# Performance work log

Measured on AMD Instinct MI355X. Metric: run time of the kernel, lower is better.

Reference implementation:

```python
import jax, jax.numpy as jnp
import numpy as np

H = 2048          # hidden_size
I = 8192          # intermediate_size (shared expert)
E = 32            # num_experts
K = 4             # num_experts_per_tok
M = 1408          # moe_intermediate_size
B, S = 2, 1024


def setup_inputs() -> dict:
    key = jax.random.key(0)
    ks = jax.random.split(key, 7)
    scale = 0.02
    return {
        "hidden_states": jax.random.normal(ks[0], (B, S, H), dtype=jnp.float32),
        "gate_w": jax.random.normal(ks[1], (H, E), dtype=jnp.float32) * scale,
        "w1": jax.random.normal(ks[2], (E, H, M), dtype=jnp.float32) * scale,  # expert up-proj
        "w2": jax.random.normal(ks[3], (E, M, H), dtype=jnp.float32) * scale,  # expert down-proj
        "ws1": jax.random.normal(ks[4], (H, I), dtype=jnp.float32) * scale,    # shared up-proj
        "ws2": jax.random.normal(ks[5], (I, H), dtype=jnp.float32) * scale,    # shared down-proj
    }


def reference(hidden_states, gate_w, w1, w2, ws1, ws2):
    b, s, h = hidden_states.shape
    x = hidden_states.reshape(-1, h)                      # [T, H]

    # shared expert: Linear -> SiLU -> Linear
    shared = jax.nn.silu(x @ ws1) @ ws2                   # [T, H]

    # router: top-k logits, softmax over the k selected logits
    router_logits = x @ gate_w                            # [T, E]
    top_vals, top_idx = jax.lax.top_k(router_logits, K)   # [T, K]
    routing_weights = jax.nn.softmax(top_vals, axis=-1)   # [T, K]

    # combine weights: scatter top-k weights into dense [T, E]
    cw = (jax.nn.one_hot(top_idx, E, dtype=x.dtype)
          * routing_weights[..., None]).sum(axis=1)       # [T, E]

    # expert FFNs (dense over experts, weighted combine)
    a = jax.nn.silu(jnp.einsum('th,ehm->tem', x, w1))     # [T, E, M]
    expert_out = jnp.einsum('tem,emh,te->th', a, w2, cw)  # [T, H]

    output = (shared + expert_out).reshape(b, s, h)
    return output, router_logits.reshape(b, s, E)
```

## Files before the change

kernel.cpp:

```cpp
#include <hip/hip_runtime.h>

#define H_ 2048
#define E_ 32
#define KSEL 4
#define M_ 1408
#define I_ 8192
#define T_ 2048

typedef __bf16 bf16;
typedef bf16 bf16x8 __attribute__((ext_vector_type(8)));
typedef float f32x4 __attribute__((ext_vector_type(4)));
typedef unsigned short u16x8 __attribute__((ext_vector_type(8)));
typedef unsigned int u32x4 __attribute__((ext_vector_type(4)));

static __device__ __forceinline__ unsigned short bfb(float f) {
  return __builtin_bit_cast(unsigned short, (bf16)f);
}

static __device__ __forceinline__ void gload_lds16(const void* g, void* l) {
  __builtin_amdgcn_global_load_lds((const __attribute__((address_space(1))) void*)g,
                                   (__attribute__((address_space(3))) void*)l, 16, 0, 0);
}

static __device__ __forceinline__ float silu_f(float v) {
  return v / (1.f + __expf(-v));
}

static __device__ __forceinline__ void wave_argmax(float& v, int& vi) {
  #pragma unroll
  for (int off = 32; off >= 1; off >>= 1) {
    float ov = __shfl_xor(v, off);
    int   oi = __shfl_xor(vi, off);
    if (ov > v || (ov == v && oi < vi)) { v = ov; vi = oi; }
  }
}

__global__ __launch_bounds__(64) void prep_k(int* __restrict__ counts) {
  if (threadIdx.x < E_) counts[threadIdx.x] = 0;
}

__global__ __launch_bounds__(256) void cvt_k(const float* __restrict__ x, unsigned short* __restrict__ xb) {
  size_t i = ((size_t)blockIdx.x * 256 + threadIdx.x) * 8;
  float4 a = *(const float4*)(x + i);
  float4 b = *(const float4*)(x + i + 4);
  u16x8 o;
  o[0]=bfb(a.x); o[1]=bfb(a.y); o[2]=bfb(a.z); o[3]=bfb(a.w);
  o[4]=bfb(b.x); o[5]=bfb(b.y); o[6]=bfb(b.z); o[7]=bfb(b.w);
  *(u16x8*)(xb + i) = o;
}

__global__ __launch_bounds__(256) void combine_k(const float* __restrict__ sc,
                                                 const float* __restrict__ sc2,
                                                 float* __restrict__ out) {
  size_t i = ((size_t)blockIdx.x * 256 + threadIdx.x) * 4;
  int t = (int)(i >> 11);
  int h = (int)(i & 2047);
  const float* s = sc + (size_t)(t * 4) * H_ + h;
  float4 a = *(const float4*)(s);
  float4 b = *(const float4*)(s + H_);
  float4 c = *(const float4*)(s + 2 * H_);
  float4 d = *(const float4*)(s + 3 * H_);
  float4 o;
  o.x = a.x + b.x + c.x + d.x;
  o.y = a.y + b.y + c.y + d.y;
  o.z = a.z + b.z + c.z + d.z;
  o.w = a.w + b.w + c.w + d.w;
  #pragma unroll
  for (int kz = 0; kz < 4; ++kz) {
    float4 v = *(const float4*)(sc2 + (size_t)kz * T_ * H_ + i);
    o.x += v.x; o.y += v.y; o.z += v.z; o.w += v.w;
  }
  *(float4*)(out + i) = o;
}

__global__ __launch_bounds__(64) void router_k(const float* __restrict__ x, const float* __restrict__ gw,
                                               float* __restrict__ logits, int* __restrict__ counts,
                                               int* __restrict__ tlist, float* __restrict__ wlist) {
  int t = blockIdx.x;
  int l = threadIdx.x;
  int e = l & 31;
  int half = l >> 5;
  const float* xr = x + (size_t)t * H_ + half * (H_/2);
  const float* g  = gw + (size_t)(half * (H_/2)) * E_ + e;
  float a0=0.f, a1=0.f, a2=0.f, a3=0.f;
  for (int h = 0; h < H_/2; h += 4) {
    a0 = fmaf(xr[h],   g[(size_t)h*E_],     a0);
    a1 = fmaf(xr[h+1], g[(size_t)(h+1)*E_], a1);
    a2 = fmaf(xr[h+2], g[(size_t)(h+2)*E_], a2);
    a3 = fmaf(xr[h+3], g[(size_t)(h+3)*E_], a3);
  }
  float acc = (a0+a1)+(a2+a3);
  acc += __shfl_xor(acc, 32);
  if (l < E_) logits[(size_t)t*E_ + l] = acc;

  float cur = (l < E_) ? acc : -INFINITY;
  int myidx = (l < E_) ? e : 1000;
  float tv0,tv1,tv2,tv3; int ti0,ti1,ti2,ti3;
  { float v=cur; int vi=myidx; wave_argmax(v,vi); tv0=v; ti0=vi; if (myidx==vi) cur=-INFINITY; }
  { float v=cur; int vi=myidx; wave_argmax(v,vi); tv1=v; ti1=vi; if (myidx==vi) cur=-INFINITY; }
  { float v=cur; int vi=myidx; wave_argmax(v,vi); tv2=v; ti2=vi; if (myidx==vi) cur=-INFINITY; }
  { float v=cur; int vi=myidx; wave_argmax(v,vi); tv3=v; ti3=vi; }
  float w0 = 1.f;
  float w1 = __expf(tv1 - tv0);
  float w2 = __expf(tv2 - tv0);
  float w3 = __expf(tv3 - tv0);
  float inv = 1.f / (w0+w1+w2+w3);
  if (l < KSEL) {
    float myw = ((l==0)?w0:(l==1)?w1:(l==2)?w2:w3) * inv;
    int   myi = ((l==0)?ti0:(l==1)?ti1:(l==2)?ti2:ti3);
    int pos = atomicAdd(&counts[myi], 1);
    tlist[myi*T_ + pos] = (t << 2) | l;
    wlist[myi*T_ + pos] = myw;
  }
}

template<int MODE, int KDIM, int NDIM, int ASTR, int KSPLIT>
__global__ __launch_bounds__(256) void gemm_k(
    const bf16* __restrict__ A, const float* __restrict__ Bf,
    bf16* __restrict__ Cb, float* __restrict__ Cf,
    const int* __restrict__ tlist, const float* __restrict__ wlist,
    const int* __restrict__ counts)
{
  __shared__ __align__(16) char smem[24576];
  char* As = smem;
  char* Bs = smem + 16384;
  const int tid = threadIdx.x;

  int mt, nt, e = 0, kz = 0;
  int nrows = T_;
  const int* lst = nullptr;
  const float* Bp = Bf;
  if constexpr (MODE == 2 || MODE == 3) {
    constexpr int NT = NDIM / 64;
    constexpr int NWG = NT * E_ * 2;
    constexpr int CPX = NWG / 8;
    int id = blockIdx.x;
    int lg = (id & 7) * CPX + (id >> 3);
    int bit = lg & 1;
    int en  = lg >> 1;
    e  = en / NT;
    nt = en % NT;
    mt = (blockIdx.y == 0) ? bit : (2 + 2*((int)blockIdx.y - 1) + bit);
    nrows = counts[e];
    if (mt * 128 >= nrows) return;
    lst = tlist + e*T_;
    Bp = Bf + (size_t)e * ((size_t)KDIM * NDIM);
  } else {
    constexpr int NWG = 16 * (NDIM / 64);
    constexpr int CPX = NWG / 8;
    int id = blockIdx.x;
    int lg = (id & 7) * CPX + (id >> 3);
    mt = lg & 15;
    nt = lg >> 4;
    if constexpr (KSPLIT > 1) kz = blockIdx.z;
  }
  const int mrow0 = mt*128, ncol0 = nt*64;

  const bf16* abase[4];
  int aoffs[4];
  #pragma unroll
  for (int c = 0; c < 4; ++c) {
    int lidx = c*256 + tid;
    int row  = lidx >> 3;
    int slot = lidx & 7;
    aoffs[c] = (slot ^ (row & 7)) * 8;
    int ri = mrow0 + row;
    if constexpr (MODE == 2) {
      int tt = (ri < nrows) ? (lst[ri] >> 2) : 0;
      abase[c] = A + (size_t)tt * ASTR;
    } else if constexpr (MODE == 3) {
      int ar = (ri < nrows) ? lst[ri] : 0;
      abase[c] = A + (size_t)ar * ASTR;
    } else {
      abase[c] = A + (size_t)ri * ASTR;
    }
  }

  const int bn = tid & 63;
  const int bq = tid >> 6;
  const float* bsrc0 = Bp + (size_t)(bq * 16) * NDIM + ncol0 + bn;
  char* const bdst = Bs + (bq*2)*1024 + bn*16;

  const int l  = tid & 63;
  const int wv = tid >> 6;
  const int wr = wv >> 1, wc = wv & 1;
  const int ss = l >> 4;

  f32x4 acc[4][2] = {};

  constexpr int ITERS = KDIM / 64 / KSPLIT;
  static_assert(ITERS % 2 == 0, "K-loop is 2-unrolled");
  const int kt0 = kz * ITERS;
  const int ktend = kt0 + ITERS;

  float vA[16], vB[16];

#define LOADB(P, KT) do {                                            \
    const float* bs_ = bsrc0 + (size_t)((KT) * 64) * NDIM;           \
    _Pragma("unroll")                                                \
    for (int j = 0; j < 16; ++j) P[j] = bs_[(size_t)j * NDIM];       \
  } while (0)

#define WRITEB(P) do {                                               \
    u32x4 lo_, hi_;                                                  \
    _Pragma("unroll")                                                \
    for (int j = 0; j < 4; ++j) {                                    \
      lo_[j] = (unsigned)bfb(P[2*j])   | ((unsigned)bfb(P[2*j+1]) << 16); \
      hi_[j] = (unsigned)bfb(P[8+2*j]) | ((unsigned)bfb(P[8+2*j+1]) << 16); \
    }                                                                \
    *(u32x4*)(bdst)        = lo_;                                    \
    *(u32x4*)(bdst + 1024) = hi_;                                    \
  } while (0)

#define MFMA_HALF(S) do {                                            \
    bf16x8 af[4], bfr[2];                                            \
    const int ks = (S)*4 + ss;                                       \
    _Pragma("unroll")                                                \
    for (int mf = 0; mf < 4; ++mf) {                                 \
      int r = wr*64 + mf*16 + (l & 15);                              \
      af[mf] = *(const bf16x8*)(As + r*128 + ((ks ^ (r & 7)) << 4)); \
    }                                                                \
    _Pragma("unroll")                                                \
    for (int nf = 0; nf < 2; ++nf) {                                 \
      int c = wc*32 + nf*16 + (l & 15);                              \
      bfr[nf] = *(const bf16x8*)(Bs + ks*1024 + c*16);               \
    }                                                                \
    _Pragma("unroll")                                                \
    for (int mf = 0; mf < 4; ++mf)                                   \
      _Pragma("unroll")                                              \
      for (int nf = 0; nf < 2; ++nf)                                 \
        acc[mf][nf] = __builtin_amdgcn_mfma_f32_16x16x32_bf16(af[mf], bfr[nf], acc[mf][nf], 0, 0, 0); \
  } while (0)

#define MFMA_PHASE() do { MFMA_HALF(0); MFMA_HALF(1); } while (0)

#define ADMA(KT) do {                                                \
    _Pragma("unroll")                                                \
    for (int c = 0; c < 4; ++c)                                      \
      gload_lds16(abase[c] + (KT)*64 + aoffs[c], As + (c*256 + tid)*16); \
  } while (0)

  LOADB(vA, kt0);
  for (int kt = kt0; kt < ktend; kt += 2) {
    __syncthreads();
    ADMA(kt);
    WRITEB(vA);
    __syncthreads();
    LOADB(vB, kt + 1);
    MFMA_PHASE();

    __syncthreads();
    ADMA(kt + 1);
    WRITEB(vB);
    __syncthreads();
    if (kt + 2 < ktend) LOADB(vA, kt + 2);
    MFMA_PHASE();
  }

#undef LOADB
#undef WRITEB
#undef MFMA_HALF
#undef MFMA_PHASE
#undef ADMA

  #pragma unroll
  for (int mf = 0; mf < 4; ++mf) {
    #pragma unroll
    for (int j = 0; j < 4; ++j) {
      const int rloc = wr*64 + mf*16 + (l >> 4)*4 + j;
      const int grow = mrow0 + rloc;
      if constexpr (MODE == 0) {
        #pragma unroll
        for (int nf = 0; nf < 2; ++nf) {
          int col = ncol0 + wc*32 + nf*16 + (l & 15);
          Cb[(size_t)grow * NDIM + col] = (bf16)silu_f(acc[mf][nf][j]);
        }
      } else if constexpr (MODE == 1) {
        float* dst = Cf + (size_t)kz * T_ * H_;
        #pragma unroll
        for (int nf = 0; nf < 2; ++nf) {
          int col = ncol0 + wc*32 + nf*16 + (l & 15);
          dst[(size_t)grow * NDIM + col] = acc[mf][nf][j];
        }
      } else if constexpr (MODE == 2) {
        if (grow < nrows) {
          int entry = lst[grow];
          float wg = wlist[e*T_ + grow];
          #pragma unroll
          for (int nf = 0; nf < 2; ++nf) {
            int col = ncol0 + wc*32 + nf*16 + (l & 15);
            Cb[(size_t)entry * NDIM + col] = (bf16)(silu_f(acc[mf][nf][j]) * wg);
          }
        }
      } else {
        if (grow < nrows) {
          int entry = lst[grow];
          #pragma unroll
          for (int nf = 0; nf < 2; ++nf) {
            int col = ncol0 + wc*32 + nf*16 + (l & 15);
            Cf[(size_t)entry * H_ + col] = acc[mf][nf][j];
          }
        }
      }
    }
  }
}

extern "C" void kernel_launch(void* const* d_in, const int* in_sizes, int n_in,
                              void* d_out, int out_size, void* d_ws, size_t ws_size,
                              hipStream_t stream) {
  const float* x   = (const float*)d_in[0];
  const float* gw  = (const float*)d_in[1];
  const float* w1  = (const float*)d_in[2];
  const float* w2  = (const float*)d_in[3];
  const float* ws1 = (const float*)d_in[4];
  const float* ws2 = (const float*)d_in[5];
  float* out    = (float*)d_out;
  float* logits = out + (size_t)T_ * H_;

  char* ws = (char*)d_ws;
  const size_t off_xb   = 0;
  const size_t off_y1   = off_xb  + (size_t)T_ * H_ * 2;
  const size_t off_act  = off_y1  + (size_t)T_ * I_ * 2;
  const size_t off_cnt  = off_act + (size_t)T_ * 4 * M_ * 2;
  const size_t off_tl   = off_cnt + 256;
  const size_t off_wl   = off_tl  + (size_t)E_ * T_ * 4;
  const size_t off_sc   = off_wl  + (size_t)E_ * T_ * 4;
  const size_t off_sc2  = off_sc  + (size_t)T_ * 4 * H_ * 4;

  const bf16* xb = (const bf16*)(ws + off_xb);
  bf16* y1  = (bf16*)(ws + off_y1);
  bf16* act = (bf16*)(ws + off_act);
  int*  counts = (int*)(ws + off_cnt);
  int*  tlist  = (int*)(ws + off_tl);
  float* wlist = (float*)(ws + off_wl);
  float* scratch  = (float*)(ws + off_sc);
  float* scratch2 = (float*)(ws + off_sc2);

  prep_k<<<1, 64, 0, stream>>>(counts);
  router_k<<<T_, 64, 0, stream>>>(x, gw, logits, counts, tlist, wlist);
  cvt_k<<<2048, 256, 0, stream>>>(x, (unsigned short*)(ws + off_xb));

  gemm_k<0, 2048, 8192, 2048, 1><<<dim3(2048), 256, 0, stream>>>(
      xb, ws1, y1, nullptr, nullptr, nullptr, nullptr);
  gemm_k<1, 8192, 2048, 8192, 4><<<dim3(512, 1, 4), 256, 0, stream>>>(
      y1, ws2, nullptr, scratch2, nullptr, nullptr, nullptr);
  gemm_k<2, 2048, 1408, 2048, 1><<<dim3(22*E_*2, 8), 256, 0, stream>>>(
      xb, w1, act, nullptr, tlist, wlist, counts);
  gemm_k<3, 1408, 2048, 1408, 1><<<dim3(32*E_*2, 8), 256, 0, stream>>>(
      act, w2, nullptr, scratch, tlist, nullptr, counts);
  combine_k<<<4096, 256, 0, stream>>>(scratch, scratch2, out);
}
```

Baseline: 807.6 us.

## Stream fp32 B tiles into LDS via async DMA and convert to bf16 there

Replaces per-thread register loads of the fp32 weight tile with global_load_lds direct-to-LDS DMA into a double-buffered fp32 staging area. Each thread then reads its column from LDS, converts it to bf16 and writes the swizzled bf16 tile that the MFMA path reads. The aim is to cut VGPR pressure and let weight loads overlap with compute asynchronously. In exchange, LDS per block grows from 24KB to 56KB, which can lower occupancy, and each tile now takes an extra LDS round-trip.

```diff
diff --git a/kernel.cpp b/kernel.cpp
--- a/kernel.cpp
+++ b/kernel.cpp
@@ -121,9 +121,10 @@
     const int* __restrict__ tlist, const float* __restrict__ wlist,
     const int* __restrict__ counts)
 {
-  __shared__ __align__(16) char smem[24576];
-  char* As = smem;
-  char* Bs = smem + 16384;
+  __shared__ __align__(16) char smem[57344];
+  char* As   = smem;
+  char* Bs32 = smem + 16384;
+  char* Bsb  = smem + 49152;
   const int tid = threadIdx.x;
 
   int mt, nt, e = 0, kz = 0;
@@ -176,10 +177,16 @@
     }
   }
 
+  const float* bbaseD[4];
+  #pragma unroll
+  for (int c = 0; c < 4; ++c) {
+    int lidx = c*256 + tid;
+    bbaseD[c] = Bp + (size_t)(lidx >> 4) * NDIM + ncol0 + (lidx & 15) * 4;
+  }
+
   const int bn = tid & 63;
   const int bq = tid >> 6;
-  const float* bsrc0 = Bp + (size_t)(bq * 16) * NDIM + ncol0 + bn;
-  char* const bdst = Bs + (bq*2)*1024 + bn*16;
+  char* const bdst = Bsb + (bq*2)*1024 + bn*16;
 
   const int l  = tid & 63;
   const int wv = tid >> 6;
@@ -193,20 +200,30 @@
   const int kt0 = kz * ITERS;
   const int ktend = kt0 + ITERS;
 
-  float vA[16], vB[16];
-
-#define LOADB(P, KT) do {                                            \
-    const float* bs_ = bsrc0 + (size_t)((KT) * 64) * NDIM;           \
-    _Pragma("unroll")                                                \
-    for (int j = 0; j < 16; ++j) P[j] = bs_[(size_t)j * NDIM];       \
+#define ADMA(KT) do {                                                \
+    _Pragma("unroll")                                                \
+    for (int c = 0; c < 4; ++c)                                      \
+      gload_lds16(abase[c] + (KT)*64 + aoffs[c], As + (c*256 + tid)*16); \
   } while (0)
 
-#define WRITEB(P) do {                                               \
+#define BDMA(KT, BUF) do {                                           \
+    _Pragma("unroll")                                                \
+    for (int c = 0; c < 4; ++c)                                      \
+      gload_lds16(bbaseD[c] + (size_t)(KT)*64*NDIM,                  \
+                  Bs32 + (BUF)*16384 + (c*256 + tid)*16);            \
+  } while (0)
+
+#define CVT(BUF) do {                                                \
+    const char* b32_ = Bs32 + (BUF)*16384;                           \
+    float f_[16];                                                    \
+    _Pragma("unroll")                                                \
+    for (int j = 0; j < 16; ++j)                                     \
+      f_[j] = *(const float*)(b32_ + (bq*16 + j)*256 + bn*4);        \
     u32x4 lo_, hi_;                                                  \
     _Pragma("unroll")                                                \
     for (int j = 0; j < 4; ++j) {                                    \
-      lo_[j] = (unsigned)bfb(P[2*j])   | ((unsigned)bfb(P[2*j+1]) << 16); \
-      hi_[j] = (unsigned)bfb(P[8+2*j]) | ((unsigned)bfb(P[8+2*j+1]) << 16); \
+      lo_[j] = (unsigned)bfb(f_[2*j])   | ((unsigned)bfb(f_[2*j+1]) << 16); \
+      hi_[j] = (unsigned)bfb(f_[8+2*j]) | ((unsigned)bfb(f_[8+2*j+1]) << 16); \
     }                                                                \
     *(u32x4*)(bdst)        = lo_;                                    \
     *(u32x4*)(bdst + 1024) = hi_;                                    \
@@ -223,7 +240,7 @@
     _Pragma("unroll")                                                \
     for (int nf = 0; nf < 2; ++nf) {                                 \
       int c = wc*32 + nf*16 + (l & 15);                              \
-      bfr[nf] = *(const bf16x8*)(Bs + ks*1024 + c*16);               \
+      bfr[nf] = *(const bf16x8*)(Bsb + ks*1024 + c*16);              \
     }                                                                \
     _Pragma("unroll")                                                \
     for (int mf = 0; mf < 4; ++mf)                                   \
@@ -234,34 +251,30 @@
 
 #define MFMA_PHASE() do { MFMA_HALF(0); MFMA_HALF(1); } while (0)
 
-#define ADMA(KT) do {                                                \
-    _Pragma("unroll")                                                \
-    for (int c = 0; c < 4; ++c)                                      \
-      gload_lds16(abase[c] + (KT)*64 + aoffs[c], As + (c*256 + tid)*16); \
-  } while (0)
-
-  LOADB(vA, kt0);
+  BDMA(kt0, 0);
+  __syncthreads();
+
   for (int kt = kt0; kt < ktend; kt += 2) {
     __syncthreads();
     ADMA(kt);
-    WRITEB(vA);
+    BDMA(kt + 1, 1);
+    CVT(0);
     __syncthreads();
-    LOADB(vB, kt + 1);
     MFMA_PHASE();
 
     __syncthreads();
     ADMA(kt + 1);
-    WRITEB(vB);
+    if (kt + 2 < ktend) BDMA(kt + 2, 0);
+    CVT(1);
     __syncthreads();
-    if (kt + 2 < ktend) LOADB(vA, kt + 2);
     MFMA_PHASE();
   }
 
-#undef LOADB
-#undef WRITEB
+#undef ADMA
+#undef BDMA
+#undef CVT
 #undef MFMA_HALF
 #undef MFMA_PHASE
-#undef ADMA
 
   #pragma unroll
   for (int mf = 0; mf < 4; ++mf) {
```

Measured after the change: 845.3 us. +4.7%, slower.

## Merge shared-expert and routed-expert GEMMs into two combined launches

Applied to the files above, without the earlier changes.

Four separate GEMM launches are replaced by two kernels. Each kernel dispatches on block index to either the routed-expert GEMM or the shared-expert GEMM of the same stage. Blocks from the two independent GEMMs can then co-run, filling the tail idle time and the many early-exit expert blocks left by sparse routing. The cost is fixed grid shapes and a possible mismatch between work ordering and block scheduling.

```diff
diff --git a/kernel.cpp b/kernel.cpp
--- a/kernel.cpp
+++ b/kernel.cpp
@@ -115,45 +115,15 @@
 }
 
 template<int MODE, int KDIM, int NDIM, int ASTR, int KSPLIT>
-__global__ __launch_bounds__(256) void gemm_k(
-    const bf16* __restrict__ A, const float* __restrict__ Bf,
+__device__ __forceinline__ void gemm_body(
+    char* __restrict__ smem, int mt, int nt, int kz, int nrows,
+    const bf16* __restrict__ A, const float* __restrict__ Bp,
     bf16* __restrict__ Cb, float* __restrict__ Cf,
-    const int* __restrict__ tlist, const float* __restrict__ wlist,
-    const int* __restrict__ counts)
+    const int* __restrict__ lst, const float* __restrict__ wl)
 {
-  __shared__ __align__(16) char smem[24576];
   char* As = smem;
   char* Bs = smem + 16384;
   const int tid = threadIdx.x;
-
-  int mt, nt, e = 0, kz = 0;
-  int nrows = T_;
-  const int* lst = nullptr;
-  const float* Bp = Bf;
-  if constexpr (MODE == 2 || MODE == 3) {
-    constexpr int NT = NDIM / 64;
-    constexpr int NWG = NT * E_ * 2;
-    constexpr int CPX = NWG / 8;
-    int id = blockIdx.x;
-    int lg = (id & 7) * CPX + (id >> 3);
-    int bit = lg & 1;
-    int en  = lg >> 1;
-    e  = en / NT;
-    nt = en % NT;
-    mt = (blockIdx.y == 0) ? bit : (2 + 2*((int)blockIdx.y - 1) + bit);
-    nrows = counts[e];
-    if (mt * 128 >= nrows) return;
-    lst = tlist + e*T_;
-    Bp = Bf + (size_t)e * ((size_t)KDIM * NDIM);
-  } else {
-    constexpr int NWG = 16 * (NDIM / 64);
-    constexpr int CPX = NWG / 8;
-    int id = blockIdx.x;
-    int lg = (id & 7) * CPX + (id >> 3);
-    mt = lg & 15;
-    nt = lg >> 4;
-    if constexpr (KSPLIT > 1) kz = blockIdx.z;
-  }
   const int mrow0 = mt*128, ncol0 = nt*64;
 
   const bf16* abase[4];
@@ -285,7 +255,7 @@
       } else if constexpr (MODE == 2) {
         if (grow < nrows) {
           int entry = lst[grow];
-          float wg = wlist[e*T_ + grow];
+          float wg = wl[grow];
           #pragma unroll
           for (int nf = 0; nf < 2; ++nf) {
             int col = ncol0 + wc*32 + nf*16 + (l & 15);
@@ -306,6 +276,73 @@
   }
 }
 
+__global__ __launch_bounds__(256) void fusedA_k(
+    const bf16* __restrict__ xb, const float* __restrict__ w1, const float* __restrict__ ws1,
+    bf16* __restrict__ act, bf16* __restrict__ y1,
+    const int* __restrict__ tlist, const float* __restrict__ wlist, const int* __restrict__ counts)
+{
+  __shared__ __align__(16) char smem[24576];
+  if (blockIdx.x < 1408) {
+    constexpr int NT = M_ / 64;
+    constexpr int NWG = NT * E_ * 2;
+    constexpr int CPX = NWG / 8;
+    int id = blockIdx.x;
+    int lg = (id & 7) * CPX + (id >> 3);
+    int bit = lg & 1;
+    int en  = lg >> 1;
+    int e  = en / NT;
+    int nt = en % NT;
+    int mt = (blockIdx.y == 0) ? bit : (2 + 2*((int)blockIdx.y - 1) + bit);
+    int nrows = counts[e];
+    if (mt * 128 >= nrows) return;
+    gemm_body<2, 2048, M_, 2048, 1>(smem, mt, nt, 0, nrows,
+        xb, w1 + (size_t)e * 2048 * M_, act, nullptr, tlist + e*T_, wlist + e*T_);
+  } else {
+    int t = ((int)blockIdx.x - 1408) * 8 + (int)blockIdx.y;
+    constexpr int CPX = 2048 / 8;
+    int lg = (t & 7) * CPX + (t >> 3);
+    int mt = lg & 15;
+    int nt = lg >> 4;
+    gemm_body<0, 2048, I_, 2048, 1>(smem, mt, nt, 0, T_,
+        xb, ws1, y1, nullptr, nullptr, nullptr);
+  }
+}
+
+__global__ __launch_bounds__(256) void fusedB_k(
+    const bf16* __restrict__ y1, const float* __restrict__ ws2,
+    const bf16* __restrict__ act, const float* __restrict__ w2,
+    float* __restrict__ scratch2, float* __restrict__ scratch,
+    const int* __restrict__ tlist, const int* __restrict__ counts)
+{
+  __shared__ __align__(16) char smem[24576];
+  if (blockIdx.x < 2048) {
+    constexpr int NT = H_ / 64;
+    constexpr int NWG = NT * E_ * 2;
+    constexpr int CPX = NWG / 8;
+    int id = blockIdx.x;
+    int lg = (id & 7) * CPX + (id >> 3);
+    int bit = lg & 1;
+    int en  = lg >> 1;
+    int e  = en / NT;
+    int nt = en % NT;
+    int mt = (blockIdx.y == 0) ? bit : (2 + 2*((int)blockIdx.y - 1) + bit);
+    int nrows = counts[e];
+    if (mt * 128 >= nrows) return;
+    gemm_body<3, M_, H_, M_, 1>(smem, mt, nt, 0, nrows,
+        act, w2 + (size_t)e * M_ * H_, nullptr, scratch, tlist + e*T_, nullptr);
+  } else {
+    int id = ((int)blockIdx.x - 2048) * 8 + (int)blockIdx.y;
+    int kz  = id & 3;
+    int sub = id >> 2;
+    constexpr int CPX = 512 / 8;
+    int lg = (sub & 7) * CPX + (sub >> 3);
+    int mt = lg & 15;
+    int nt = lg >> 4;
+    gemm_body<1, I_, H_, I_, 4>(smem, mt, nt, kz, T_,
+        y1, ws2, nullptr, scratch2, nullptr, nullptr);
+  }
+}
+
 extern "C" void kernel_launch(void* const* d_in, const int* in_sizes, int n_in,
                               void* d_out, int out_size, void* d_ws, size_t ws_size,
                               hipStream_t stream) {
@@ -341,13 +378,9 @@
   router_k<<<T_, 64, 0, stream>>>(x, gw, logits, counts, tlist, wlist);
   cvt_k<<<2048, 256, 0, stream>>>(x, (unsigned short*)(ws + off_xb));
 
-  gemm_k<0, 2048, 8192, 2048, 1><<<dim3(2048), 256, 0, stream>>>(
-      xb, ws1, y1, nullptr, nullptr, nullptr, nullptr);
-  gemm_k<1, 8192, 2048, 8192, 4><<<dim3(512, 1, 4), 256, 0, stream>>>(
-      y1, ws2, nullptr, scratch2, nullptr, nullptr, nullptr);
-  gemm_k<2, 2048, 1408, 2048, 1><<<dim3(22*E_*2, 8), 256, 0, stream>>>(
-      xb, w1, act, nullptr, tlist, wlist, counts);
-  gemm_k<3, 1408, 2048, 1408, 1><<<dim3(32*E_*2, 8), 256, 0, stream>>>(
-      act, w2, nullptr, scratch, tlist, nullptr, counts);
+  fusedA_k<<<dim3(1408 + 256, 8), 256, 0, stream>>>(
+      xb, w1, ws1, act, y1, tlist, wlist, counts);
+  fusedB_k<<<dim3(2048 + 256, 8), 256, 0, stream>>>(
+      y1, ws2, act, w2, scratch2, scratch, tlist, counts);
   combine_k<<<4096, 256, 0, stream>>>(scratch, scratch2, out);
 }
```

Result: faster. 741.4 us (-8.2%).
